# Optimization experiments

Measured on AMD Instinct MI355X. Metric: run time of the kernel, lower is better.

The kernel has to match this reference:

```python
import jax, jax.numpy as jnp
import numpy as np

BN_EPS = 1e-5


def _conv2d(x, w, pad):
    # x: [B,C,H,W], w: [O,I,kh,kw]
    return jax.lax.conv_general_dilated(
        x, w, window_strides=(1, 1), padding=((pad, pad), (pad, pad)),
        dimension_numbers=("NCHW", "OIHW", "NCHW"))


def _feat(x, conv_w, bn_gamma, bn_beta, bn_mean, bn_var, desc_w, desc_b):
    # BasicConv(64->32, k=3, pad=1): conv (no bias) -> BN (inference) -> ReLU
    y = _conv2d(x, conv_w, pad=1)
    inv = bn_gamma / jnp.sqrt(bn_var + BN_EPS)
    y = y * inv[None, :, None, None] + (bn_beta - bn_mean * inv)[None, :, None, None]
    y = jnp.maximum(y, 0.0)
    # desc: 1x1 conv 32->32 with bias
    y = _conv2d(y, desc_w, pad=0) + desc_b[None, :, None, None]
    return y  # [B,32,H,W]


def setup_inputs() -> dict:
    key = jax.random.key(0)
    ks = jax.random.split(key, 4)
    B, Cin, H, W = 8, 64, 160, 576
    left = jax.random.normal(ks[0], (B, Cin, H, W), dtype=jnp.float32)
    right = jax.random.normal(ks[1], (B, Cin, H, W), dtype=jnp.float32)
    conv_w = jax.random.normal(ks[2], (32, 64, 3, 3), dtype=jnp.float32) * 0.05
    bn_gamma = jnp.ones((32,), jnp.float32)
    bn_beta = jnp.zeros((32,), jnp.float32)
    bn_mean = jnp.zeros((32,), jnp.float32)
    bn_var = jnp.ones((32,), jnp.float32)
    desc_w = jax.random.normal(ks[3], (32, 32, 1, 1), dtype=jnp.float32) * 0.1
    desc_b = jnp.zeros((32,), jnp.float32)
    return {"left": left, "right": right, "conv_w": conv_w,
            "bn_gamma": bn_gamma, "bn_beta": bn_beta,
            "bn_mean": bn_mean, "bn_var": bn_var,
            "desc_w": desc_w, "desc_b": desc_b, "maxdisp": 48}


def reference(left, right, conv_w, bn_gamma, bn_beta, bn_mean, bn_var,
              desc_w, desc_b, maxdisp):
    L = _feat(left, conv_w, bn_gamma, bn_beta, bn_mean, bn_var, desc_w, desc_b)
    R = _feat(right, conv_w, bn_gamma, bn_beta, bn_mean, bn_var, desc_w, desc_b)
    # reduce_mean is a frozen 1x1 conv with weight 1/32 == mean over channels.
    cv = [jnp.mean(L * R, axis=1)]  # d = 0, [B,H,W]
    for d in range(1, maxdisp):  # maxdisp is a static Python int (structural)
        c = jnp.mean(L[:, :, :, d:] * R[:, :, :, :-d], axis=1)  # [B,H,W-d]
        cv.append(jnp.pad(c, ((0, 0), (0, 0), (d, 0))))  # zero-pad left edge
    return jnp.stack(cv, axis=1)  # [B, maxdisp, H, W]
```

## Files before the change

kernel.cpp:

```cpp
#include <hip/hip_runtime.h>
#include <stdint.h>

#define HH   160
#define WW   576
#define CIN  64
#define BATCH 8
#define MAXD 48

typedef unsigned int  uint;
typedef unsigned short ushort;
typedef __attribute__((ext_vector_type(8))) short bf16x8;
typedef __attribute__((ext_vector_type(4))) float f32x4;
typedef __attribute__((ext_vector_type(16))) float f32x16;

static constexpr size_t WTB_OFF  = 0;
static constexpr size_t DWT_OFF  = 36864;
static constexpr size_t B1_OFF   = 38912;
static constexpr size_t B2_OFF   = 39040;
static constexpr size_t FEAT_OFF = 40960;
static constexpr size_t FEAT_ELEMS = (size_t)BATCH * HH * WW * 32;

__device__ __forceinline__ uint f2bf(float f) {
    uint u = __float_as_uint(f);
    u = (u + 0x7fffu + ((u >> 16) & 1u)) >> 16;
    return u;
}
__device__ __forceinline__ float bf2f_lo(uint u) { return __uint_as_float(u << 16); }
__device__ __forceinline__ float bf2f_hi(uint u) { return __uint_as_float(u & 0xffff0000u); }
__device__ __forceinline__ uint pk2(float a, float b) { return f2bf(a) | (f2bf(b) << 16); }
__device__ __forceinline__ float elem4(float4 f, int k) {
    return k == 0 ? f.x : k == 1 ? f.y : k == 2 ? f.z : f.w;
}

__global__ void prep_kernel(const float* __restrict__ conv_w,
                            const float* __restrict__ gamma,
                            const float* __restrict__ beta,
                            const float* __restrict__ mean,
                            const float* __restrict__ var,
                            const float* __restrict__ desc_w,
                            const float* __restrict__ desc_b,
                            char* __restrict__ ws) {
    int tid = blockIdx.x * 256 + threadIdx.x;
    ushort* wtB = (ushort*)(ws + WTB_OFF);
    ushort* dwt = (ushort*)(ws + DWT_OFF);
    float*  b1  = (float*)(ws + B1_OFF);
    float*  b2  = (float*)(ws + B2_OFF);
    if (tid < 36 * 64 * 8) {
        int j    = tid & 7;
        int l    = (tid >> 3) & 63;
        int f    = tid >> 9;
        int s    = f & 3;
        int tap  = f >> 2;
        int ch = l & 31;
        int ci = s * 16 + (l >> 5) * 8 + j;
        float inv = gamma[ch] * rsqrtf(var[ch] + 1e-5f);
        wtB[tid] = (ushort)f2bf(conv_w[(size_t)(ch * 64 + ci) * 9 + tap] * inv);
    }
    if (tid < 1024) {
        int j = tid & 7;
        int l = (tid >> 3) & 63;
        int s = tid >> 9;
        int o = l & 31;
        int mid = (j & 3) + 8 * (j >> 2) + 16 * s + 4 * (l >> 5);
        dwt[tid] = (ushort)f2bf(desc_w[o * 32 + mid]);
    }
    if (tid < 32) {
        float inv = gamma[tid] * rsqrtf(var[tid] + 1e-5f);
        b1[tid] = beta[tid] - mean[tid] * inv;
        b2[tid] = desc_b[tid];
    }
}

#define NXB 6
#define NYB 40
#define NWG (NXB * NYB * 2 * BATCH)
__global__ __launch_bounds__(256, 4)
void feat_mfma(const float* __restrict__ left,
               const float* __restrict__ right,
               const char* __restrict__ ws,
               ushort* __restrict__ featL,
               ushort* __restrict__ featR) {
    __shared__ __align__(16) ushort tile[600 * 32];

    int bid = blockIdx.x;
    int nid = (bid & 7) * (NWG / 8) + (bid >> 3);
    int x    = nid % NXB;
    int rest = nid / NXB;
    int hy   = rest % NYB;
    int z    = rest / NYB;
    int b    = z & 7;
    const float* __restrict__ in = (z < 8 ? left : right) + (size_t)b * CIN * HH * WW;
    ushort* __restrict__ feat = (z < 8 ? featL : featR);
    const int w0 = x * 96;
    const int h0 = hy * 4;
    const int PL = HH * WW;

    const int lane = threadIdx.x & 63;
    const int wv   = threadIdx.x >> 6;
    const int n    = lane & 31;
    const int hi   = lane >> 5;

    const ushort* __restrict__ wtB = (const ushort*)(ws + WTB_OFF);

    f32x16 acc[3] = {};

    for (int chunk = 0; chunk < 2; ++chunk) {
        for (int t = threadIdx.x; t < 768; t += 256) {
            int oct = t / 192;
            int rem = t - oct * 192;
            int r   = rem >> 5;
            int g   = rem & 31;
            if (g <= 25) {
                int gh  = h0 + r - 1;
                int gw4 = w0 - 4 + g * 4;
                float4 v[8];
                if (((unsigned)gh < HH) && ((unsigned)gw4 < WW)) {
                    const float* src = in + (size_t)(chunk * 32 + oct * 8) * PL
                                          + (size_t)gh * WW + gw4;
#pragma unroll
                    for (int j = 0; j < 8; ++j)
                        v[j] = *(const float4*)(src + (size_t)j * PL);
                } else {
#pragma unroll
                    for (int j = 0; j < 8; ++j) v[j] = make_float4(0.f, 0.f, 0.f, 0.f);
                }
#pragma unroll
                for (int k = 0; k < 4; ++k) {
                    int c = g * 4 + k - 3;
                    if (c < 0 || c > 97) continue;
                    uint4 o4;
                    o4.x = pk2(elem4(v[0], k), elem4(v[1], k));
                    o4.y = pk2(elem4(v[2], k), elem4(v[3], k));
                    o4.z = pk2(elem4(v[4], k), elem4(v[5], k));
                    o4.w = pk2(elem4(v[6], k), elem4(v[7], k));
                    int px = r * 100 + c;
                    *(uint4*)&tile[(size_t)px * 32 + ((oct ^ ((px >> 2) & 3)) * 8)] = o4;
                }
            }
        }
        __syncthreads();

#pragma unroll
        for (int tap = 0; tap < 9; ++tap) {
            const int r = tap / 3, kw = tap % 3;
#pragma unroll
            for (int s = 0; s < 2; ++s) {
                const int S = chunk * 2 + s;
                bf16x8 a = *(const bf16x8*)(wtB + (size_t)((tap * 4 + S) * 64 + lane) * 8);
#pragma unroll
                for (int tl = 0; tl < 3; ++tl) {
                    int px = (wv + r) * 100 + tl * 32 + n + kw;
                    bf16x8 bb = *(const bf16x8*)&tile[(size_t)px * 32 +
                                   (((2 * s + hi) ^ ((px >> 2) & 3)) * 8)];
                    acc[tl] = __builtin_amdgcn_mfma_f32_32x32x16_bf16(a, bb, acc[tl], 0, 0, 0);
                }
            }
        }
        __syncthreads();
    }

    const float* __restrict__ b1 = (const float*)(ws + B1_OFF);
    const float* __restrict__ b2 = (const float*)(ws + B2_OFF);
    f32x4 b1q[4], b2q[4];
#pragma unroll
    for (int q = 0; q < 4; ++q) {
        b1q[q] = *(const f32x4*)(b1 + 8 * q + 4 * hi);
        b2q[q] = *(const f32x4*)(b2 + 8 * q + 4 * hi);
    }
    const ushort* __restrict__ dwt = (const ushort*)(ws + DWT_OFF);
    bf16x8 da0 = *(const bf16x8*)(dwt + (size_t)lane * 8);
    bf16x8 da1 = *(const bf16x8*)(dwt + (size_t)(64 + lane) * 8);

#pragma unroll
    for (int tl = 0; tl < 3; ++tl) {
        bf16x8 p0, p1;
#pragma unroll
        for (int j = 0; j < 8; ++j) {
            float v0 = fmaxf(acc[tl][j]     + b1q[j >> 2][j & 3],       0.f);
            float v1 = fmaxf(acc[tl][8 + j] + b1q[2 + (j >> 2)][j & 3], 0.f);
            p0[j] = (short)f2bf(v0);
            p1[j] = (short)f2bf(v1);
        }
        f32x16 acc2;
#pragma unroll
        for (int j = 0; j < 16; ++j) acc2[j] = b2q[j >> 2][j & 3];
        acc2 = __builtin_amdgcn_mfma_f32_32x32x16_bf16(da0, p0, acc2, 0, 0, 0);
        acc2 = __builtin_amdgcn_mfma_f32_32x32x16_bf16(da1, p1, acc2, 0, 0, 0);

        size_t pix = ((size_t)b * HH + h0 + wv) * WW + w0 + tl * 32 + n;
        ushort* fp = feat + pix * 32 + 4 * hi;
#pragma unroll
        for (int q = 0; q < 4; ++q) {
            uint u0 = pk2(acc2[4 * q],     acc2[4 * q + 1]);
            uint u1 = pk2(acc2[4 * q + 2], acc2[4 * q + 3]);
            *(uint2*)(fp + 8 * q) = make_uint2(u0, u1);
        }
    }
}

#define CVT 192
__global__ __launch_bounds__(CVT)
void cv_kernel(const ushort* __restrict__ featL,
               const ushort* __restrict__ featR,
               float* __restrict__ out) {
    __shared__ ushort r_lds[WW * 40];

    const int t  = threadIdx.x;
    const int bh = blockIdx.x;
    const int b  = bh / HH;
    const int h  = bh - b * HH;
    const ushort* __restrict__ Lrow = featL + ((size_t)b * HH + h) * WW * 32;
    const ushort* __restrict__ Rrow = featR + ((size_t)b * HH + h) * WW * 32;

#pragma unroll
    for (int k = 0; k < 3; ++k) {
        int w = t + k * CVT;
        const uint4* src = (const uint4*)(Rrow + (size_t)w * 32);
        uint4* dst = (uint4*)(r_lds + (size_t)w * 40);
#pragma unroll
        for (int j = 0; j < 4; ++j) dst[j] = src[j];
    }

    float Lf[3][32];
#pragma unroll
    for (int k = 0; k < 3; ++k) {
        int w = t + k * CVT;
        const uint4* src = (const uint4*)(Lrow + (size_t)w * 32);
#pragma unroll
        for (int j = 0; j < 4; ++j) {
            uint4 v = src[j];
            uint vv[4] = {v.x, v.y, v.z, v.w};
#pragma unroll
            for (int q = 0; q < 4; ++q) {
                Lf[k][j * 8 + q * 2]     = bf2f_lo(vv[q]);
                Lf[k][j * 8 + q * 2 + 1] = bf2f_hi(vv[q]);
            }
        }
    }
    __syncthreads();

    float* __restrict__ outBase = out + ((size_t)b * MAXD * HH + h) * WW;
    for (int d = 0; d < MAXD; ++d) {
#pragma unroll
        for (int k = 0; k < 3; ++k) {
            int w = t + k * CVT;
            float res = 0.f;
            if (w >= d) {
                const uint4* rp = (const uint4*)(r_lds + (size_t)(w - d) * 40);
                float s0 = 0.f, s1 = 0.f;
#pragma unroll
                for (int j = 0; j < 4; ++j) {
                    uint4 v = rp[j];
                    uint vv[4] = {v.x, v.y, v.z, v.w};
#pragma unroll
                    for (int q = 0; q < 4; ++q) {
                        int idx = j * 8 + q * 2;
                        s0 = fmaf(Lf[k][idx],     bf2f_lo(vv[q]), s0);
                        s1 = fmaf(Lf[k][idx + 1], bf2f_hi(vv[q]), s1);
                    }
                }
                res = (s0 + s1) * (1.f / 32.f);
            }
            outBase[(size_t)d * HH * WW + w] = res;
        }
    }
}

extern "C" void kernel_launch(void* const* d_in, const int* in_sizes, int n_in,
                              void* d_out, int out_size, void* d_ws, size_t ws_size,
                              hipStream_t stream) {
    const float* left   = (const float*)d_in[0];
    const float* right  = (const float*)d_in[1];
    const float* conv_w = (const float*)d_in[2];
    const float* gamma  = (const float*)d_in[3];
    const float* beta   = (const float*)d_in[4];
    const float* mean   = (const float*)d_in[5];
    const float* var    = (const float*)d_in[6];
    const float* desc_w = (const float*)d_in[7];
    const float* desc_b = (const float*)d_in[8];
    float*  out   = (float*)d_out;
    char*   ws    = (char*)d_ws;
    ushort* featL = (ushort*)(ws + FEAT_OFF);
    ushort* featR = featL + FEAT_ELEMS;

    prep_kernel<<<72, 256, 0, stream>>>(conv_w, gamma, beta, mean, var, desc_w, desc_b, ws);
    feat_mfma<<<NWG, 256, 0, stream>>>(left, right, ws, featL, featR);
    cv_kernel<<<BATCH * HH, CVT, 0, stream>>>(featL, featR, out);
}
```

Measured before the change: 235.5 us.

## Shrink LDS tile to 16-channel chunks with scalar loads for higher occupancy

The feature conv kernel now stages 16 input channels per chunk (four chunks instead of two), which cuts the LDS tile to a quarter of its previous size. Each thread loads one pixel across eight channels with scalar loads instead of float4 vectors, and the XOR swizzle is dropped in favour of a plain two-plane layout. Launch bounds go from 4 to 6 waves-per-SIMD hint, aiming for more resident blocks to hide global-load latency. In exchange the kernel issues more, narrower global loads and twice as many barrier syncs, and the unswizzled LDS reads may hit bank conflicts.

```diff
diff --git a/kernel.cpp b/kernel.cpp
--- a/kernel.cpp
+++ b/kernel.cpp
@@ -28,9 +28,6 @@
 __device__ __forceinline__ float bf2f_lo(uint u) { return __uint_as_float(u << 16); }
 __device__ __forceinline__ float bf2f_hi(uint u) { return __uint_as_float(u & 0xffff0000u); }
 __device__ __forceinline__ uint pk2(float a, float b) { return f2bf(a) | (f2bf(b) << 16); }
-__device__ __forceinline__ float elem4(float4 f, int k) {
-    return k == 0 ? f.x : k == 1 ? f.y : k == 2 ? f.z : f.w;
-}
 
 __global__ void prep_kernel(const float* __restrict__ conv_w,
                             const float* __restrict__ gamma,
@@ -74,13 +71,13 @@
 #define NXB 6
 #define NYB 40
 #define NWG (NXB * NYB * 2 * BATCH)
-__global__ __launch_bounds__(256, 4)
+__global__ __launch_bounds__(256, 6)
 void feat_mfma(const float* __restrict__ left,
                const float* __restrict__ right,
                const char* __restrict__ ws,
                ushort* __restrict__ featL,
                ushort* __restrict__ featR) {
-    __shared__ __align__(16) ushort tile[600 * 32];
+    __shared__ __align__(16) ushort tile[2 * 600 * 8];
 
     int bid = blockIdx.x;
     int nid = (bid & 7) * (NWG / 8) + (bid >> 3);
@@ -104,38 +101,37 @@
 
     f32x16 acc[3] = {};
 
-    for (int chunk = 0; chunk < 2; ++chunk) {
-        for (int t = threadIdx.x; t < 768; t += 256) {
-            int oct = t / 192;
-            int rem = t - oct * 192;
-            int r   = rem >> 5;
-            int g   = rem & 31;
-            if (g <= 25) {
-                int gh  = h0 + r - 1;
-                int gw4 = w0 - 4 + g * 4;
-                float4 v[8];
-                if (((unsigned)gh < HH) && ((unsigned)gw4 < WW)) {
-                    const float* src = in + (size_t)(chunk * 32 + oct * 8) * PL
-                                          + (size_t)gh * WW + gw4;
-#pragma unroll
-                    for (int j = 0; j < 8; ++j)
-                        v[j] = *(const float4*)(src + (size_t)j * PL);
-                } else {
-#pragma unroll
-                    for (int j = 0; j < 8; ++j) v[j] = make_float4(0.f, 0.f, 0.f, 0.f);
+    for (int chunk = 0; chunk < 4; ++chunk) {
+        for (int t = threadIdx.x; t < 1536; t += 256) {
+            int lpx  = t & 63;
+            int seg  = t >> 6;
+            int part = seg & 1;
+            int oct  = (seg >> 1) & 1;
+            int r    = seg >> 2;
+            int px   = part * 64 + lpx;
+            if (px < 100) {
+                int gh = h0 + r - 1;
+                int gw = w0 - 1 + px;
+                float f0 = 0.f, f1 = 0.f, f2 = 0.f, f3 = 0.f,
+                      f4 = 0.f, f5 = 0.f, f6 = 0.f, f7 = 0.f;
+                if (((unsigned)gh < HH) && ((unsigned)gw < WW)) {
+                    const float* src = in + (size_t)(chunk * 16 + oct * 8) * PL
+                                          + (size_t)gh * WW + gw;
+                    f0 = src[0];
+                    f1 = src[(size_t)PL];
+                    f2 = src[(size_t)2 * PL];
+                    f3 = src[(size_t)3 * PL];
+                    f4 = src[(size_t)4 * PL];
+                    f5 = src[(size_t)5 * PL];
+                    f6 = src[(size_t)6 * PL];
+                    f7 = src[(size_t)7 * PL];
                 }
-#pragma unroll
-                for (int k = 0; k < 4; ++k) {
-                    int c = g * 4 + k - 3;
-                    if (c < 0 || c > 97) continue;
-                    uint4 o4;
-                    o4.x = pk2(elem4(v[0], k), elem4(v[1], k));
-                    o4.y = pk2(elem4(v[2], k), elem4(v[3], k));
-                    o4.z = pk2(elem4(v[4], k), elem4(v[5], k));
-                    o4.w = pk2(elem4(v[6], k), elem4(v[7], k));
-                    int px = r * 100 + c;
-                    *(uint4*)&tile[(size_t)px * 32 + ((oct ^ ((px >> 2) & 3)) * 8)] = o4;
-                }
+                uint4 o4;
+                o4.x = pk2(f0, f1);
+                o4.y = pk2(f2, f3);
+                o4.z = pk2(f4, f5);
+                o4.w = pk2(f6, f7);
+                *(uint4*)&tile[(size_t)(oct * 600 + r * 100 + px) * 8] = o4;
             }
         }
         __syncthreads();
@@ -143,17 +139,12 @@
 #pragma unroll
         for (int tap = 0; tap < 9; ++tap) {
             const int r = tap / 3, kw = tap % 3;
-#pragma unroll
-            for (int s = 0; s < 2; ++s) {
-                const int S = chunk * 2 + s;
-                bf16x8 a = *(const bf16x8*)(wtB + (size_t)((tap * 4 + S) * 64 + lane) * 8);
-#pragma unroll
-                for (int tl = 0; tl < 3; ++tl) {
-                    int px = (wv + r) * 100 + tl * 32 + n + kw;
-                    bf16x8 bb = *(const bf16x8*)&tile[(size_t)px * 32 +
-                                   (((2 * s + hi) ^ ((px >> 2) & 3)) * 8)];
-                    acc[tl] = __builtin_amdgcn_mfma_f32_32x32x16_bf16(a, bb, acc[tl], 0, 0, 0);
-                }
+            bf16x8 a = *(const bf16x8*)(wtB + (size_t)((tap * 4 + chunk) * 64 + lane) * 8);
+#pragma unroll
+            for (int tl = 0; tl < 3; ++tl) {
+                int px = (wv + r) * 100 + tl * 32 + n + kw;
+                bf16x8 bb = *(const bf16x8*)&tile[(size_t)(hi * 600 + px) * 8];
+                acc[tl] = __builtin_amdgcn_mfma_f32_32x32x16_bf16(a, bb, acc[tl], 0, 0, 0);
             }
         }
         __syncthreads();
```

Measured after the change: 416.1 us. 1.77x slower.
